# Kernel optimization log

Hardware: AMD Instinct MI355X
Metric: run time of the kernel (lower is better)

## Reference

```python
import jax, jax.numpy as jnp
import numpy as np
import math

DIM_K = 64  # head dim used for scaling
NEG = -1000000000.0

def setup_inputs() -> dict:
    key = jax.random.key(0)
    k1, k2, k3, k4 = jax.random.split(key, 4)
    B, H, S, D = 4, 16, 2048, 64
    return {
        "key": jax.random.normal(k1, (B, H, S, D), dtype=jnp.float32),
        "query": jax.random.normal(k2, (B, H, S, D), dtype=jnp.float32),
        "value": jax.random.normal(k3, (B, H, S, D), dtype=jnp.float32),
        "mask": jax.random.randint(k4, (B, S, S), 0, 2, dtype=jnp.int32),
    }

def reference(key, query, value, mask):
    # scores: [B,H,Sq,Sk]
    scores = jnp.einsum('bhqd,bhkd->bhqk', query, key) / math.sqrt(DIM_K)
    scores = jnp.where(mask[:, None, :, :] == 0, NEG, scores)
    attn = jax.nn.softmax(scores, axis=-1)  # dropout is identity in eval mode
    return jnp.einsum('bhqk,bhkd->bhqd', attn, value)
```

## Files before the change

kernel.cpp:

```cpp
#include <hip/hip_runtime.h>
#include <stdint.h>

#define B_ 4
#define H_ 16
#define S_ 2048
#define D_ 64
#define NKT (S_ / 64)
#define QM 128

typedef __attribute__((ext_vector_type(8))) short bf16x8;
typedef __attribute__((ext_vector_type(4))) float f32x4;
typedef unsigned long long u64;
typedef unsigned int u32;

__device__ inline short f2bf(float f) {
  union { float f; u32 u; } x; x.f = f;
  u32 r = x.u + 0x7FFFu + ((x.u >> 16) & 1u);
  return (short)(r >> 16);
}
__device__ inline short4 f2bf4(float4 v) {
  short4 s; s.x = f2bf(v.x); s.y = f2bf(v.y); s.z = f2bf(v.z); s.w = f2bf(v.w);
  return s;
}
__device__ inline short f2bf_fast(float f) {
  union { float f; u32 u; } x; x.f = f;
  return (short)((x.u + 0x8000u) >> 16);
}

__device__ inline int SW(int row, int byteoff) {
  return row * 128 + (byteoff ^ ((row & 7) << 4));
}

__device__ inline void gll16(const void* g, void* l) {
  __builtin_amdgcn_global_load_lds(
      (const __attribute__((address_space(1))) u32*)g,
      (__attribute__((address_space(3))) u32*)(uintptr_t)l, 16, 0, 0);
}

__global__ __launch_bounds__(256)
void prepass(const float* __restrict__ Kg, const float* __restrict__ Vg,
             const int* __restrict__ Mg,
             char* __restrict__ Ksw, char* __restrict__ Vsw, u64* __restrict__ Mp) {
  __shared__ short tile[4096];
  const int bid = blockIdx.x, tid = threadIdx.x;
  if (bid < 8192) {
    int idx = bid * 256 + tid;
    int row = idx >> 4, c4 = idx & 15;
    float4 v = *(const float4*)(Kg + (size_t)idx * 4);
    *(short4*)(Ksw + (size_t)row * 128 + ((c4 * 8) ^ ((row & 7) << 4))) = f2bf4(v);
  } else if (bid < 10240) {
    int vb = bid - 8192;
    char* ct = (char*)tile;
    int c4 = tid & 15, g = tid >> 4;
    const float* src = Vg + (size_t)vb * (64 * D_) + (size_t)(g * 4) * D_ + c4 * 4;
    float4 vv[4];
#pragma unroll
    for (int i = 0; i < 4; ++i) vv[i] = *(const float4*)(src + (size_t)i * D_);
    const float* vf = (const float*)vv;
#pragma unroll
    for (int dd = 0; dd < 4; ++dd) {
      short4 s;
      s.x = f2bf(vf[0 * 4 + dd]);
      s.y = f2bf(vf[1 * 4 + dd]);
      s.z = f2bf(vf[2 * 4 + dd]);
      s.w = f2bf(vf[3 * 4 + dd]);
      *(short4*)(ct + SW(c4 * 4 + dd, g * 8)) = s;
    }
    __syncthreads();
    char* dst = Vsw + (size_t)vb * 8192;
#pragma unroll
    for (int j = 0; j < 2; ++j)
      *(float4*)(dst + tid * 16 + j * 4096) = *(const float4*)(ct + tid * 16 + j * 4096);
  } else {
    int pb = bid - 10240;
    int gbase = pb * 1024;
#pragma unroll
    for (int j = 0; j < 4; ++j) {
      int idx = gbase + j * 256 + tid;
      u64 bits = __ballot(Mg[idx] != 0);
      if ((tid & 63) == 0) Mp[idx >> 6] = bits;
    }
  }
}

__global__ __launch_bounds__(256, 3)
void attn_kernel(const float* __restrict__ Qg,
                 const char* __restrict__ Ksw,
                 const char* __restrict__ Vsw,
                 const u64* __restrict__ Mp,
                 float* __restrict__ Og) {
  __shared__ short sK[2][4096];
  __shared__ short sV[2][4096];
  __shared__ short sP[8192];

  const int tid  = threadIdx.x;
  const int w    = tid >> 6;
  const int lane = tid & 63;
  const int quad = lane >> 4;
  const int c    = lane & 15;
  const int bh   = blockIdx.y;
  const int b    = bh >> 4;
  const int q0   = blockIdx.x * QM;
  const size_t base = (size_t)bh * (S_ * D_);
  const char* Kt = Ksw + (size_t)bh * (S_ * 128);
  const char* Vt = Vsw + (size_t)bh * (S_ * 128);
  char* cP = (char*)sP;

  const float SC = 0.125f * 1.44269504088896f;
#pragma unroll
  for (int j = 0; j < 8; ++j) {
    int idx = tid + j * 256;
    int row = idx >> 4, c4 = idx & 15;
    float4 v = *(const float4*)(Qg + base + (size_t)(q0 + row) * D_ + c4 * 4);
    v.x *= SC; v.y *= SC; v.z *= SC; v.w *= SC;
    *(short4*)(cP + SW(row, c4 * 8)) = f2bf4(v);
  }
#pragma unroll
  for (int j = 0; j < 2; ++j) {
    gll16(Kt + tid * 16 + j * 4096, (char*)sK[0] + tid * 16 + j * 4096);
    gll16(Vt + tid * 16 + j * 4096, (char*)sV[0] + tid * 16 + j * 4096);
  }
  __syncthreads();

  bf16x8 qa[2][2];
#pragma unroll
  for (int gi = 0; gi < 2; ++gi) {
    qa[gi][0] = *(bf16x8*)(cP + SW(32 * w + 16 * gi + c, quad * 16));
    qa[gi][1] = *(bf16x8*)(cP + SW(32 * w + 16 * gi + c, 64 + quad * 16));
  }

  f32x4 acco[2][4];
  float l_part[2][4];
#pragma unroll
  for (int gi = 0; gi < 2; ++gi)
#pragma unroll
    for (int i = 0; i < 4; ++i) { acco[gi][i] = f32x4{0,0,0,0}; l_part[gi][i] = 0.f; }

  const u64* mrow[2];
  mrow[0] = Mp + ((size_t)b * S_ + q0 + 32 * w + quad * 4) * NKT;
  mrow[1] = mrow[0] + 16 * NKT;

  u64 mw[2][4];
#pragma unroll
  for (int gi = 0; gi < 2; ++gi)
#pragma unroll
    for (int r = 0; r < 4; ++r) mw[gi][r] = mrow[gi][(size_t)r * NKT];

  for (int kt = 0; kt < NKT; ++kt) {
    const char* cK = (const char*)sK[kt & 1];
    const char* cV = (const char*)sV[kt & 1];

    __syncthreads();

    if (kt + 1 < NKT) {
      char* kn = (char*)sK[(kt + 1) & 1];
      char* vn = (char*)sV[(kt + 1) & 1];
      const char* kg = Kt + (size_t)(kt + 1) * 8192;
      const char* vg = Vt + (size_t)(kt + 1) * 8192;
#pragma unroll
      for (int j = 0; j < 2; ++j) {
        gll16(kg + tid * 16 + j * 4096, kn + tid * 16 + j * 4096);
        gll16(vg + tid * 16 + j * 4096, vn + tid * 16 + j * 4096);
      }
    }
    const int ktn = (kt + 1 < NKT) ? kt + 1 : kt;
    u64 mwn[2][4];
#pragma unroll
    for (int gi = 0; gi < 2; ++gi)
#pragma unroll
      for (int r = 0; r < 4; ++r) mwn[gi][r] = mrow[gi][(size_t)r * NKT + ktn];

    f32x4 accs[2][4];
#pragma unroll
    for (int n = 0; n < 4; ++n) {
      bf16x8 kb0 = *(bf16x8*)(cK + SW(16 * n + c, quad * 16));
      bf16x8 kb1 = *(bf16x8*)(cK + SW(16 * n + c, 64 + quad * 16));
#pragma unroll
      for (int gi = 0; gi < 2; ++gi) {
        f32x4 z = {0, 0, 0, 0};
        z = __builtin_amdgcn_mfma_f32_16x16x32_bf16(qa[gi][0], kb0, z, 0, 0, 0);
        z = __builtin_amdgcn_mfma_f32_16x16x32_bf16(qa[gi][1], kb1, z, 0, 0, 0);
        accs[gi][n] = z;
      }
    }

#pragma unroll
    for (int gi = 0; gi < 2; ++gi) {
#pragma unroll
      for (int r = 0; r < 4; ++r) {
        unsigned mlo = (unsigned)(mw[gi][r]) >> c;
        unsigned mhi = (unsigned)(mw[gi][r] >> 32) >> c;
        float e0 = (mlo & 1u)         ? exp2f(accs[gi][0][r]) : 0.0f;
        float e1 = ((mlo >> 16) & 1u) ? exp2f(accs[gi][1][r]) : 0.0f;
        float e2 = (mhi & 1u)         ? exp2f(accs[gi][2][r]) : 0.0f;
        float e3 = ((mhi >> 16) & 1u) ? exp2f(accs[gi][3][r]) : 0.0f;
        l_part[gi][r] += (e0 + e1) + (e2 + e3);
        int prow = 32 * w + 16 * gi + quad * 4 + r;
        *(short*)(cP + SW(prow, (c) * 2))      = f2bf_fast(e0);
        *(short*)(cP + SW(prow, (16 + c) * 2)) = f2bf_fast(e1);
        *(short*)(cP + SW(prow, (32 + c) * 2)) = f2bf_fast(e2);
        *(short*)(cP + SW(prow, (48 + c) * 2)) = f2bf_fast(e3);
      }
    }
#pragma unroll
    for (int gi = 0; gi < 2; ++gi)
#pragma unroll
      for (int r = 0; r < 4; ++r) mw[gi][r] = mwn[gi][r];

    bf16x8 pa[2][2];
#pragma unroll
    for (int gi = 0; gi < 2; ++gi) {
      pa[gi][0] = *(bf16x8*)(cP + SW(32 * w + 16 * gi + c, quad * 16));
      pa[gi][1] = *(bf16x8*)(cP + SW(32 * w + 16 * gi + c, 64 + quad * 16));
    }

#pragma unroll
    for (int dn = 0; dn < 4; ++dn) {
      bf16x8 vb0 = *(bf16x8*)(cV + SW(16 * dn + c, quad * 16));
      bf16x8 vb1 = *(bf16x8*)(cV + SW(16 * dn + c, 64 + quad * 16));
#pragma unroll
      for (int gi = 0; gi < 2; ++gi) {
        acco[gi][dn] = __builtin_amdgcn_mfma_f32_16x16x32_bf16(pa[gi][0], vb0, acco[gi][dn], 0, 0, 0);
        acco[gi][dn] = __builtin_amdgcn_mfma_f32_16x16x32_bf16(pa[gi][1], vb1, acco[gi][dn], 0, 0, 0);
      }
    }
  }

#pragma unroll
  for (int gi = 0; gi < 2; ++gi) {
#pragma unroll
    for (int r = 0; r < 4; ++r) {
      float l = l_part[gi][r];
      l += __shfl_xor(l, 1);
      l += __shfl_xor(l, 2);
      l += __shfl_xor(l, 4);
      l += __shfl_xor(l, 8);
      float inv = 1.0f / l;
      size_t orow = base + (size_t)(q0 + 32 * w + 16 * gi + quad * 4 + r) * D_;
#pragma unroll
      for (int dn = 0; dn < 4; ++dn)
        Og[orow + 16 * dn + c] = acco[gi][dn][r] * inv;
    }
  }
}

extern "C" void kernel_launch(void* const* d_in, const int* in_sizes, int n_in,
                              void* d_out, int out_size, void* d_ws, size_t ws_size,
                              hipStream_t stream) {
  const float* Kg = (const float*)d_in[0];
  const float* Qg = (const float*)d_in[1];
  const float* Vg = (const float*)d_in[2];
  const int*   Mg = (const int*)d_in[3];
  float* Og = (float*)d_out;

  char* ws  = (char*)d_ws;
  u64*  Mp  = (u64*)ws;
  char* Ksw = ws + (size_t)(2u << 20);
  char* Vsw = ws + (size_t)(2u << 20) + (16u << 20);

  prepass<<<26624, 256, 0, stream>>>(Kg, Vg, Mg, Ksw, Vsw, Mp);
  attn_kernel<<<dim3(S_ / QM, B_ * H_), 256, 0, stream>>>(Qg, Ksw, Vsw, Mp, Og);
}
```

Measured before the change: 332.8 us.

## Shrink P scratch to per-wave strips to fit four blocks per CU

The shared P buffer is cut from a full 128-row tile to a 16-row strip per wave, reused for both 16-row groups, and the initial Q staging now goes through the K buffer. Together with raising the launch-bounds occupancy hint from 3 to 4, this lowers LDS use per block so more blocks can be resident to hide latency. It also switches the P bf16 conversion to packed round-to-nearest intrinsics, splits the row-sum accumulators into float2 pairs, and unrolls the key-tile loop by 2. The tighter register budget at 4 blocks per CU risks spills, and the extra syncs around Q staging add a little prologue cost.

After: 532.7 us. 1.6x slower.

```diff
diff --git a/kernel.cpp b/kernel.cpp
--- a/kernel.cpp
+++ b/kernel.cpp
@@ -1,4 +1,5 @@
 #include <hip/hip_runtime.h>
+#include <hip/hip_bf16.h>
 #include <stdint.h>
 
 #define B_ 4
@@ -21,10 +22,6 @@
 __device__ inline short4 f2bf4(float4 v) {
   short4 s; s.x = f2bf(v.x); s.y = f2bf(v.y); s.z = f2bf(v.z); s.w = f2bf(v.w);
   return s;
-}
-__device__ inline short f2bf_fast(float f) {
-  union { float f; u32 u; } x; x.f = f;
-  return (short)((x.u + 0x8000u) >> 16);
 }
 
 __device__ inline int SW(int row, int byteoff) {
@@ -83,7 +80,7 @@
   }
 }
 
-__global__ __launch_bounds__(256, 3)
+__global__ __launch_bounds__(256, 4)
 void attn_kernel(const float* __restrict__ Qg,
                  const char* __restrict__ Ksw,
                  const char* __restrict__ Vsw,
@@ -91,7 +88,7 @@
                  float* __restrict__ Og) {
   __shared__ short sK[2][4096];
   __shared__ short sV[2][4096];
-  __shared__ short sP[8192];
+  __shared__ short sP[4096];
 
   const int tid  = threadIdx.x;
   const int w    = tid >> 6;
@@ -104,7 +101,8 @@
   const size_t base = (size_t)bh * (S_ * D_);
   const char* Kt = Ksw + (size_t)bh * (S_ * 128);
   const char* Vt = Vsw + (size_t)bh * (S_ * 128);
-  char* cP = (char*)sP;
+  char* cK0 = (char*)sK;
+  char* strip = (char*)sP + w * 2048;
 
   const float SC = 0.125f * 1.44269504088896f;
 #pragma unroll
@@ -113,28 +111,29 @@
     int row = idx >> 4, c4 = idx & 15;
     float4 v = *(const float4*)(Qg + base + (size_t)(q0 + row) * D_ + c4 * 4);
     v.x *= SC; v.y *= SC; v.z *= SC; v.w *= SC;
-    *(short4*)(cP + SW(row, c4 * 8)) = f2bf4(v);
-  }
+    *(short4*)(cK0 + SW(row, c4 * 8)) = f2bf4(v);
+  }
+  __syncthreads();
+  bf16x8 qa[2][2];
+#pragma unroll
+  for (int gi = 0; gi < 2; ++gi) {
+    qa[gi][0] = *(bf16x8*)(cK0 + SW(32 * w + 16 * gi + c, quad * 16));
+    qa[gi][1] = *(bf16x8*)(cK0 + SW(32 * w + 16 * gi + c, 64 + quad * 16));
+  }
+  __syncthreads();
+
 #pragma unroll
   for (int j = 0; j < 2; ++j) {
     gll16(Kt + tid * 16 + j * 4096, (char*)sK[0] + tid * 16 + j * 4096);
     gll16(Vt + tid * 16 + j * 4096, (char*)sV[0] + tid * 16 + j * 4096);
   }
-  __syncthreads();
-
-  bf16x8 qa[2][2];
-#pragma unroll
-  for (int gi = 0; gi < 2; ++gi) {
-    qa[gi][0] = *(bf16x8*)(cP + SW(32 * w + 16 * gi + c, quad * 16));
-    qa[gi][1] = *(bf16x8*)(cP + SW(32 * w + 16 * gi + c, 64 + quad * 16));
-  }
 
   f32x4 acco[2][4];
-  float l_part[2][4];
+  float2 l2[2][4];
 #pragma unroll
   for (int gi = 0; gi < 2; ++gi)
 #pragma unroll
-    for (int i = 0; i < 4; ++i) { acco[gi][i] = f32x4{0,0,0,0}; l_part[gi][i] = 0.f; }
+    for (int i = 0; i < 4; ++i) { acco[gi][i] = f32x4{0,0,0,0}; l2[gi][i] = make_float2(0.f, 0.f); }
 
   const u64* mrow[2];
   mrow[0] = Mp + ((size_t)b * S_ + q0 + 32 * w + quad * 4) * NKT;
@@ -146,6 +145,7 @@
 #pragma unroll
     for (int r = 0; r < 4; ++r) mw[gi][r] = mrow[gi][(size_t)r * NKT];
 
+#pragma unroll 2
   for (int kt = 0; kt < NKT; ++kt) {
     const char* cK = (const char*)sK[kt & 1];
     const char* cV = (const char*)sV[kt & 1];
@@ -184,6 +184,7 @@
       }
     }
 
+    bf16x8 pa[2][2];
 #pragma unroll
     for (int gi = 0; gi < 2; ++gi) {
 #pragma unroll
@@ -194,25 +195,25 @@
         float e1 = ((mlo >> 16) & 1u) ? exp2f(accs[gi][1][r]) : 0.0f;
         float e2 = (mhi & 1u)         ? exp2f(accs[gi][2][r]) : 0.0f;
         float e3 = ((mhi >> 16) & 1u) ? exp2f(accs[gi][3][r]) : 0.0f;
-        l_part[gi][r] += (e0 + e1) + (e2 + e3);
-        int prow = 32 * w + 16 * gi + quad * 4 + r;
-        *(short*)(cP + SW(prow, (c) * 2))      = f2bf_fast(e0);
-        *(short*)(cP + SW(prow, (16 + c) * 2)) = f2bf_fast(e1);
-        *(short*)(cP + SW(prow, (32 + c) * 2)) = f2bf_fast(e2);
-        *(short*)(cP + SW(prow, (48 + c) * 2)) = f2bf_fast(e3);
-      }
+        float2 s01 = make_float2(e0, e1), s23 = make_float2(e2, e3);
+        l2[gi][r].x += s01.x + s23.x;
+        l2[gi][r].y += s01.y + s23.y;
+        union { __hip_bfloat162 h; short s[2]; } p01, p23;
+        p01.h = __float22bfloat162_rn(s01);
+        p23.h = __float22bfloat162_rn(s23);
+        int prow = quad * 4 + r;
+        *(short*)(strip + SW(prow, (c) * 2))      = p01.s[0];
+        *(short*)(strip + SW(prow, (16 + c) * 2)) = p01.s[1];
+        *(short*)(strip + SW(prow, (32 + c) * 2)) = p23.s[0];
+        *(short*)(strip + SW(prow, (48 + c) * 2)) = p23.s[1];
+      }
+      pa[gi][0] = *(bf16x8*)(strip + SW(c, quad * 16));
+      pa[gi][1] = *(bf16x8*)(strip + SW(c, 64 + quad * 16));
     }
 #pragma unroll
     for (int gi = 0; gi < 2; ++gi)
 #pragma unroll
       for (int r = 0; r < 4; ++r) mw[gi][r] = mwn[gi][r];
-
-    bf16x8 pa[2][2];
-#pragma unroll
-    for (int gi = 0; gi < 2; ++gi) {
-      pa[gi][0] = *(bf16x8*)(cP + SW(32 * w + 16 * gi + c, quad * 16));
-      pa[gi][1] = *(bf16x8*)(cP + SW(32 * w + 16 * gi + c, 64 + quad * 16));
-    }
 
 #pragma unroll
     for (int dn = 0; dn < 4; ++dn) {
@@ -230,7 +231,7 @@
   for (int gi = 0; gi < 2; ++gi) {
 #pragma unroll
     for (int r = 0; r < 4; ++r) {
-      float l = l_part[gi][r];
+      float l = l2[gi][r].x + l2[gi][r].y;
       l += __shfl_xor(l, 1);
       l += __shfl_xor(l, 2);
       l += __shfl_xor(l, 4);
```
